# Kernel tuning notes

Hardware: AMD Instinct MI355X
Metric: run time of the kernel (lower is better)

## Reference

```python
import jax, jax.numpy as jnp
import numpy as np

T = 5          # temporal_window_size
B = 512        # batch (graphs per timestep)
NA = 16        # num_agents (nodes per graph)
S = 64         # num_belief_states
A = 16         # action_dim
HID = 64       # hidden_dim per head
H = 4          # num_attn_heads
FD = HID * H   # 256, feature_dim
LAT = 128      # latent_dim
N = B * NA     # total nodes per timestep
FIN = S + A    # node feature dim
NEG_SLOPE = 0.2


def _edge_index():
    i, j = np.meshgrid(np.arange(NA), np.arange(NA), indexing='ij')
    m = i != j
    src_l, dst_l = i[m], j[m]                      # 240 intra-clique edges
    off = (np.arange(B) * NA)[:, None]
    src = (src_l[None] + off).ravel()
    dst = (dst_l[None] + off).ravel()
    loops = np.arange(N)                           # PyG GATConv add_self_loops=True
    src = np.concatenate([src, loops])
    dst = np.concatenate([dst, loops])
    return jnp.asarray(np.stack([src, dst]), dtype=jnp.int64)


def setup_inputs() -> dict:
    key = jax.random.key(0)
    ks = jax.random.split(key, 24)
    xav = lambda k, shp: jax.random.normal(k, shp, jnp.float32) * np.float32(np.sqrt(2.0 / (shp[0] + shp[-1])))
    return {
        'signals': jax.random.normal(ks[0], (T, B, S), jnp.float32),
        'neighbor_actions': jax.random.normal(ks[1], (T, B, NA * A), jnp.float32),
        'lin_w0': xav(ks[2], (FD, FIN)),
        'att_src0': xav(ks[3], (H, HID)),
        'att_dst0': xav(ks[4], (H, HID)),
        'bias0': jnp.zeros((FD,), jnp.float32),
        'lin_w1': xav(ks[5], (FD, FD)),
        'att_src1': xav(ks[6], (H, HID)),
        'att_dst1': xav(ks[7], (H, HID)),
        'bias1': jnp.zeros((FD,), jnp.float32),
        'in_proj_w': xav(ks[8], (3 * FD, FD)),
        'in_proj_b': jnp.zeros((3 * FD,), jnp.float32),
        'out_proj_w': xav(ks[9], (FD, FD)),
        'out_proj_b': jnp.zeros((FD,), jnp.float32),
        'w_mean': xav(ks[10], (LAT, FD)),
        'b_mean': jnp.zeros((LAT,), jnp.float32),
        'w_logvar': xav(ks[11], (LAT, FD)),
        'b_logvar': jnp.zeros((LAT,), jnp.float32),
        'w_belief': xav(ks[12], (S, FD)),
        'b_belief': jnp.zeros((S,), jnp.float32),
        'edge_index': _edge_index(),
    }


def _segment_softmax(e, seg, num_segments):
    # e: [E, T, H]; softmax over edges sharing the same target node.
    m = jax.ops.segment_max(e, seg, num_segments=num_segments)
    e = jnp.exp(e - m[seg])
    s = jax.ops.segment_sum(e, seg, num_segments=num_segments)
    return e / s[seg]


def _gat(x, src, dst, w, a_src, a_dst, b):
    # x: [N, T, Fin] -> [N, T, H*HID]   (PyG GATConv, concat heads)
    xl = jnp.einsum('ntf,of->nto', x, w).reshape(N, T, H, HID)
    e_src = jnp.einsum('nthc,hc->nth', xl, a_src)[src]   # [E, T, H]
    e_dst = jnp.einsum('nthc,hc->nth', xl, a_dst)[dst]
    e = jax.nn.leaky_relu(e_src + e_dst, NEG_SLOPE)
    alpha = _segment_softmax(e, dst, N)                  # per-target softmax
    out = jax.ops.segment_sum(alpha[..., None] * xl[src], dst, num_segments=N)
    return out.reshape(N, T, FD) + b


def reference(signals, neighbor_actions, lin_w0, att_src0, att_dst0, bias0,
              lin_w1, att_src1, att_dst1, bias1, in_proj_w, in_proj_b,
              out_proj_w, out_proj_b, w_mean, b_mean, w_logvar, b_logvar,
              w_belief, b_belief, edge_index):
    # --- _construct_graph (vectorized over time window + batch) ---
    acts = neighbor_actions.reshape(T, B, NA, A)
    beliefs = jnp.zeros((T, B, NA, S), signals.dtype).at[:, :, 0, :].set(signals)
    nodes = jnp.concatenate([beliefs, acts], -1).reshape(T, N, FIN)
    nodes = jnp.transpose(nodes, (1, 0, 2))              # [N, T, FIN]
    src, dst = edge_index[0], edge_index[1]
    x = jax.nn.relu(_gat(nodes, src, dst, lin_w0, att_src0, att_dst0, bias0))
    x = jax.nn.relu(_gat(x, src, dst, lin_w1, att_src1, att_dst1, bias1))
    # --- ego-node sequence: nodes 0, NA, 2*NA, ... ---
    seq = x[::NA]                                        # [B, T, FD]
    # --- temporal MultiheadAttention (batch_first, eval) ---
    qkv = seq @ in_proj_w.T + in_proj_b
    q, k, v = jnp.split(qkv, 3, axis=-1)
    dh = FD // H
    q = q.reshape(B, T, H, dh); k = k.reshape(B, T, H, dh); v = v.reshape(B, T, H, dh)
    scores = jnp.einsum('bqhd,bkhd->bhqk', q, k) / jnp.sqrt(jnp.asarray(dh, seq.dtype))
    # torch float attn_mask is ADDITIVE: mask[i,j]=1 if j<=i else 0
    mask = (jnp.arange(T)[:, None] >= jnp.arange(T)[None, :]).astype(seq.dtype)
    attn = jax.nn.softmax(scores + mask[None, None], axis=-1)
    ctx = jnp.einsum('bhqk,bkhd->bqhd', attn, v).reshape(B, T, FD)
    ctx = ctx @ out_proj_w.T + out_proj_b
    feat = ctx[:, -1]                                    # [B, FD]
    # --- heads ---
    mean = feat @ w_mean.T + b_mean
    logvar = feat @ w_logvar.T + b_logvar
    belief = jax.nn.softmax(feat @ w_belief.T + b_belief, axis=-1)
    return (mean, logvar, belief)
```

## Files before the change

### kernel.cpp

```cpp
#include <hip/hip_runtime.h>
#include <hip/hip_bf16.h>


__device__ __forceinline__ float wave_sum64(float v) {
    #pragma unroll
    for (int off = 32; off > 0; off >>= 1) v += __shfl_xor(v, off, 64);
    return v;
}
__device__ __forceinline__ float wave_max64(float v) {
    #pragma unroll
    for (int off = 32; off > 0; off >>= 1) v = fmaxf(v, __shfl_xor(v, off, 64));
    return v;
}

__global__ __launch_bounds__(256) void k_pre(
    const float* __restrict__ w0, const float* __restrict__ w1,
    const float* __restrict__ wip, const float* __restrict__ wop,
    const float* __restrict__ wm, const float* __restrict__ wlv,
    const float* __restrict__ wb,
    const float* __restrict__ as0, const float* __restrict__ ad0,
    const float* __restrict__ as1, const float* __restrict__ ad1,
    float* __restrict__ tws,
    float* __restrict__ u1, float* __restrict__ ud1,
    float* __restrict__ pa0, float* __restrict__ pd0)
{
    const int tid = threadIdx.x;
    if (blockIdx.x < 1680) {
        int i = blockIdx.x * 256 + tid;
        float v;
        if (i < 16384) {
            int k = i >> 8, n = i & 255;
            v = w0[n * 80 + k];
        } else if (i < 20480) {
            int j = i - 16384; int k = j >> 8, n = j & 255;
            v = w0[n * 80 + 64 + k];
        } else if (i < 86016) {
            int j = i - 20480; int k = j >> 8, n = j & 255;
            v = w1[n * 256 + k];
        } else if (i < 282624) {
            int j = i - 86016; int k = j / 768, n = j - k * 768;
            v = wip[n * 256 + k];
        } else if (i < 348160) {
            int j = i - 282624; int k = j >> 8, n = j & 255;
            v = wop[n * 256 + k];
        } else {
            int j = i - 348160; int k = j / 320, o = j - k * 320;
            if (o < 128)      v = wm[o * 256 + k];
            else if (o < 256) v = wlv[(o - 128) * 256 + k];
            else              v = wb[(o - 256) * 256 + k];
        }
        tws[i] = v;
        return;
    }
    for (int q = 0; q < 4; q++) {
        int idx = q * 256 + tid;
        int h = idx >> 8, k = idx & 255;
        float su = 0.f, sd = 0.f;
        for (int c = 0; c < 64; c++) {
            float wv = w1[(h * 64 + c) * 256 + k];
            su = fmaf(as1[h * 64 + c], wv, su);
            sd = fmaf(ad1[h * 64 + c], wv, sd);
        }
        u1[idx] = su; ud1[idx] = sd;
    }
    if (tid < 64) {
        int h = tid >> 4, k = tid & 15;
        float su = 0.f, sd = 0.f;
        for (int c = 0; c < 64; c++) {
            float wv = w0[(h * 64 + c) * 80 + 64 + k];
            su = fmaf(as0[h * 64 + c], wv, su);
            sd = fmaf(ad0[h * 64 + c], wv, sd);
        }
        pa0[tid] = su; pd0[tid] = sd;
    }
}

__global__ __launch_bounds__(256, 4) void k_gat(
    const float* __restrict__ sig,
    const float* __restrict__ nact,
    const float* __restrict__ W0sT,
    const float* __restrict__ W0aT,
    const float* __restrict__ W1T,
    const float* __restrict__ u1g, const float* __restrict__ ud1g,
    const float* __restrict__ pa0g, const float* __restrict__ pd0g,
    const float* __restrict__ as0, const float* __restrict__ ad0,
    const float* __restrict__ b0, const float* __restrict__ b1,
    float* __restrict__ seqf)
{
    __shared__ __align__(16) char smem[37120];
    float* actL    = (float*)(smem + 0);
    float* sigL    = (float*)(smem + 1024);
    float* u1L     = (float*)(smem + 1280);
    float* ud1L    = (float*)(smem + 5440);
    float* pa0L    = (float*)(smem + 9600);
    float* pd0L    = (float*)(smem + 9856);
    float* es0w    = (float*)(smem + 10112);
    float* ed0w    = (float*)(smem + 10368);
    float* espL    = (float*)(smem + 10624);
    float* es1L    = (float*)(smem + 11648);
    float* edpL    = (float*)(smem + 11904);
    float* alpha1L = (float*)(smem + 11968);
    float* a0L     = (float*)(smem + 12224);
    float* zL      = (float*)(smem + 16320);
    float* x1L     = (float*)(smem + 20480);

    const int tid = threadIdx.x;
    const int bg = blockIdx.x;
    const int b = bg / 5, g = bg - b * 5;
    const int n = tid, w = tid >> 6, lane = tid & 63;

    if (tid < 64) sigL[tid] = sig[(g * 512 + b) * 64 + tid];
    actL[tid] = nact[(g * 512 + b) * 256 + tid];
    #pragma unroll
    for (int q = 0; q < 4; q++) {
        int idx = q * 256 + tid;
        int h = idx >> 8, k = idx & 255;
        u1L[h * 260 + k] = u1g[idx];
        ud1L[h * 260 + k] = ud1g[idx];
    }
    if (tid >= 64 && tid < 128) {
        pa0L[tid - 64] = pa0g[tid - 64];
        pd0L[tid - 64] = pd0g[tid - 64];
    }
    __syncthreads();

    float S = 0.f;
    {
        const float4* sig4 = (const float4*)sigL;
        #pragma unroll
        for (int i = 0; i < 4; i++) {
            float wv[16];
            #pragma unroll
            for (int j = 0; j < 16; j++)
                wv[j] = W0sT[(i * 16 + j) * 256 + n];
            #pragma unroll
            for (int q = 0; q < 4; q++) {
                float4 sv = sig4[i * 4 + q];
                S = fmaf(wv[q * 4 + 0], sv.x, S);
                S = fmaf(wv[q * 4 + 1], sv.y, S);
                S = fmaf(wv[q * 4 + 2], sv.z, S);
                S = fmaf(wv[q * 4 + 3], sv.w, S);
            }
        }
    }
    const float sS = wave_sum64(S * as0[n]);
    const float dS = wave_sum64(S * ad0[n]);

    if (lane < 16) {
        const int m = lane;
        float su = (m == 0) ? sS : 0.f;
        float sd = (m == 0) ? dS : 0.f;
        const float4* act4 = (const float4*)(actL + m * 16);
        const float4* pa4  = (const float4*)(pa0L + w * 16);
        const float4* pd4  = (const float4*)(pd0L + w * 16);
        #pragma unroll
        for (int q = 0; q < 4; q++) {
            float4 av = act4[q], pv = pa4[q], dv = pd4[q];
            su = fmaf(av.x, pv.x, su); su = fmaf(av.y, pv.y, su);
            su = fmaf(av.z, pv.z, su); su = fmaf(av.w, pv.w, su);
            sd = fmaf(av.x, dv.x, sd); sd = fmaf(av.y, dv.y, sd);
            sd = fmaf(av.z, dv.z, sd); sd = fmaf(av.w, dv.w, sd);
        }
        es0w[w * 16 + m] = su;
        ed0w[w * 16 + m] = sd;
    }
    if (lane < 16) {
        const int j = lane;
        float ej = ed0w[w * 16 + j];
        float e[16], m = -1e30f;
        const float4* es4 = (const float4*)(es0w + w * 16);
        #pragma unroll
        for (int s4 = 0; s4 < 4; s4++) {
            float4 ev = es4[s4];
            float x;
            x = ev.x + ej; x = (x >= 0.f) ? x : 0.2f * x; e[s4*4+0] = x; m = fmaxf(m, x);
            x = ev.y + ej; x = (x >= 0.f) ? x : 0.2f * x; e[s4*4+1] = x; m = fmaxf(m, x);
            x = ev.z + ej; x = (x >= 0.f) ? x : 0.2f * x; e[s4*4+2] = x; m = fmaxf(m, x);
            x = ev.w + ej; x = (x >= 0.f) ? x : 0.2f * x; e[s4*4+3] = x; m = fmaxf(m, x);
        }
        float sum = 0.f;
        #pragma unroll
        for (int s = 0; s < 16; s++) { e[s] = __expf(e[s] - m); sum += e[s]; }
        float inv = 1.f / sum;
        float4* a04 = (float4*)(a0L + w * 256 + j * 16);
        #pragma unroll
        for (int s4 = 0; s4 < 4; s4++)
            a04[s4] = make_float4(e[s4 * 4] * inv, e[s4 * 4 + 1] * inv,
                                  e[s4 * 4 + 2] * inv, e[s4 * 4 + 3] * inv);
    }

    float x1r[16];
    {
        float wr[16];
        #pragma unroll
        for (int k = 0; k < 16; k++) wr[k] = W0aT[k * 256 + n];
        const float4* act4 = (const float4*)actL;
        float xl0r[16];
        #pragma unroll
        for (int s = 0; s < 16; s++) {
            float a = 0.f;
            #pragma unroll
            for (int q = 0; q < 4; q++) {
                float4 av = act4[s * 4 + q];
                a = fmaf(av.x, wr[q * 4 + 0], a);
                a = fmaf(av.y, wr[q * 4 + 1], a);
                a = fmaf(av.z, wr[q * 4 + 2], a);
                a = fmaf(av.w, wr[q * 4 + 3], a);
            }
            xl0r[s] = a;
        }
        xl0r[0] += S;
        const float b0v = b0[n];
        const float4* a04 = (const float4*)(a0L + w * 256);
        #pragma unroll
        for (int j = 0; j < 16; j++) {
            float acc = b0v;
            #pragma unroll
            for (int s4 = 0; s4 < 4; s4++) {
                float4 a4 = a04[j * 4 + s4];
                acc = fmaf(a4.x, xl0r[s4 * 4 + 0], acc);
                acc = fmaf(a4.y, xl0r[s4 * 4 + 1], acc);
                acc = fmaf(a4.z, xl0r[s4 * 4 + 2], acc);
                acc = fmaf(a4.w, xl0r[s4 * 4 + 3], acc);
            }
            x1r[j] = fmaxf(acc, 0.f);
            x1L[j * 260 + n] = x1r[j];
        }
    }
    __syncthreads();

    {
        const int m = tid & 15, h = (tid >> 4) & 3, p = tid >> 6;
        const float4* x4p = (const float4*)(x1L + m * 260 + p * 64);
        const float4* u4p = (const float4*)(u1L + h * 260 + p * 64);
        float a = 0.f;
        #pragma unroll
        for (int i = 0; i < 16; i++) {
            float4 xv = x4p[i], uv = u4p[i];
            a = fmaf(xv.x, uv.x, a);
            a = fmaf(xv.y, uv.y, a);
            a = fmaf(xv.z, uv.z, a);
            a = fmaf(xv.w, uv.w, a);
        }
        espL[m * 16 + h * 4 + p] = a;
        if (m == 0) {
            const float4* ud4p = (const float4*)(ud1L + h * 260 + p * 64);
            float ad = 0.f;
            #pragma unroll
            for (int i = 0; i < 16; i++) {
                float4 xv = x4p[i], uv = ud4p[i];
                ad = fmaf(xv.x, uv.x, ad);
                ad = fmaf(xv.y, uv.y, ad);
                ad = fmaf(xv.z, uv.z, ad);
                ad = fmaf(xv.w, uv.w, ad);
            }
            edpL[h * 4 + p] = ad;
        }
    }
    __syncthreads();

    if (w == 0) {
        {
            const int m = lane >> 2, h = lane & 3;
            const float* e = espL + m * 16 + h * 4;
            es1L[m * 4 + h] = e[0] + e[1] + e[2] + e[3];
        }
        if (lane < 4) {
            const int h = lane;
            float ej = edpL[h * 4] + edpL[h * 4 + 1] + edpL[h * 4 + 2] + edpL[h * 4 + 3];
            float e[16], m = -1e30f;
            #pragma unroll
            for (int s = 0; s < 16; s++) {
                float x = es1L[s * 4 + h] + ej;
                x = (x >= 0.f) ? x : 0.2f * x;
                e[s] = x; m = fmaxf(m, x);
            }
            float sum = 0.f;
            #pragma unroll
            for (int s = 0; s < 16; s++) { e[s] = __expf(e[s] - m); sum += e[s]; }
            float inv = 1.f / sum;
            #pragma unroll
            for (int s = 0; s < 16; s++) alpha1L[h * 16 + s] = e[s] * inv;
        }
    }
    __syncthreads();

    {
        const float4* a14 = (const float4*)alpha1L;
        #pragma unroll
        for (int hh = 0; hh < 4; hh++) {
            float zv = 0.f;
            #pragma unroll
            for (int s4 = 0; s4 < 4; s4++) {
                float4 a4 = a14[hh * 4 + s4];
                zv = fmaf(a4.x, x1r[s4 * 4 + 0], zv);
                zv = fmaf(a4.y, x1r[s4 * 4 + 1], zv);
                zv = fmaf(a4.z, x1r[s4 * 4 + 2], zv);
                zv = fmaf(a4.w, x1r[s4 * 4 + 3], zv);
            }
            zL[hh * 260 + n] = zv;
        }
    }
    __syncthreads();

    {
        const float4* zh = (const float4*)(zL + w * 260);
        float acc = b1[n];
        for (int i = 0; i < 16; i++) {
            float wv[16];
            #pragma unroll
            for (int j = 0; j < 16; j++)
                wv[j] = W1T[(i * 16 + j) * 256 + n];
            #pragma unroll
            for (int q = 0; q < 4; q++) {
                float4 z4 = zh[i * 4 + q];
                acc = fmaf(wv[q * 4 + 0], z4.x, acc);
                acc = fmaf(wv[q * 4 + 1], z4.y, acc);
                acc = fmaf(wv[q * 4 + 2], z4.z, acc);
                acc = fmaf(wv[q * 4 + 3], z4.w, acc);
            }
        }
        seqf[bg * 256 + n] = fmaxf(acc, 0.f);
    }
}

__global__ __launch_bounds__(768) void k_stage2(
    const float* __restrict__ seqf,
    const float* __restrict__ wipT,
    const float* __restrict__ bip,
    const float* __restrict__ wopT,
    const float* __restrict__ bop,
    const float* __restrict__ whT,
    const float* __restrict__ bm, const float* __restrict__ blv,
    const float* __restrict__ bb,
    float* __restrict__ out)
{
    __shared__ float sseq[2][5][256];
    __shared__ float kL[2][5][256], vL[2][5][256], qL[2][256];
    __shared__ float ctxL[2][256], featL[2][256];
    __shared__ float beliefL[2][64];
    const int tid = threadIdx.x;
    const int b0 = blockIdx.x * 2;

    {
        float* sflat = &sseq[0][0][0];
        for (int i = tid; i < 2560; i += 768)
            sflat[i] = seqf[b0 * 1280 + i];
    }
    __syncthreads();

    {
        const int kind = tid >> 8, n = tid & 255;
        if (kind == 0) {
            float a0 = 0.f, a1 = 0.f;
            for (int k = 0; k < 256; k++) {
                float wv = wipT[k * 768 + n];
                a0 = fmaf(sseq[0][4][k], wv, a0);
                a1 = fmaf(sseq[1][4][k], wv, a1);
            }
            float bv = bip[n];
            qL[0][n] = a0 + bv; qL[1][n] = a1 + bv;
        } else {
            const float* wcol = wipT + kind * 256 + n;
            float acc[2][5];
            #pragma unroll
            for (int gb = 0; gb < 2; gb++)
                #pragma unroll
                for (int t = 0; t < 5; t++) acc[gb][t] = 0.f;
            for (int k = 0; k < 256; k++) {
                float wv = wcol[k * 768];
                #pragma unroll
                for (int gb = 0; gb < 2; gb++) {
                    #pragma unroll
                    for (int t = 0; t < 5; t++)
                        acc[gb][t] = fmaf(sseq[gb][t][k], wv, acc[gb][t]);
                }
            }
            float bv = bip[kind * 256 + n];
            float* dst = (kind == 1) ? &kL[0][0][0] : &vL[0][0][0];
            #pragma unroll
            for (int gb = 0; gb < 2; gb++)
                #pragma unroll
                for (int t = 0; t < 5; t++)
                    dst[gb * 1280 + t * 256 + n] = acc[gb][t] + bv;
        }
    }
    __syncthreads();

    if (tid < 512) {
        const int gb = tid >> 8, col = tid & 255;
        float q4 = qL[gb][col];
        float sc[5];
        #pragma unroll
        for (int t = 0; t < 5; t++)
            sc[t] = wave_sum64(q4 * kL[gb][t][col]) * 0.125f;
        float m = sc[0];
        #pragma unroll
        for (int t = 1; t < 5; t++) m = fmaxf(m, sc[t]);
        float p[5], sum = 0.f;
        #pragma unroll
        for (int t = 0; t < 5; t++) { p[t] = __expf(sc[t] - m); sum += p[t]; }
        float inv = 1.f / sum, cv = 0.f;
        #pragma unroll
        for (int t = 0; t < 5; t++) cv = fmaf(p[t], vL[gb][t][col], cv);
        ctxL[gb][col] = cv * inv;
    }
    __syncthreads();

    if (tid < 512) {
        const int gb = tid >> 8, n = tid & 255;
        float acc = 0.f;
        for (int k = 0; k < 256; k++)
            acc = fmaf(ctxL[gb][k], wopT[k * 256 + n], acc);
        featL[gb][n] = acc + bop[n];
    }
    __syncthreads();

    if (tid < 640) {
        const int gb = tid / 320, j = tid - gb * 320;
        float acc = 0.f;
        for (int k = 0; k < 256; k++)
            acc = fmaf(featL[gb][k], whT[k * 320 + j], acc);
        if (j < 128) {
            out[(b0 + gb) * 128 + j] = acc + bm[j];
        } else if (j < 256) {
            out[65536 + (b0 + gb) * 128 + (j - 128)] = acc + blv[j - 128];
        } else {
            beliefL[gb][j - 256] = acc + bb[j - 256];
        }
    }
    __syncthreads();

    if (tid < 128) {
        int gb = tid >> 6, lane = tid & 63;
        float lg = beliefL[gb][lane];
        float m = wave_max64(lg);
        float e = __expf(lg - m);
        float s = wave_sum64(e);
        out[131072 + (b0 + gb) * 64 + lane] = e / s;
    }
}

extern "C" void kernel_launch(void* const* d_in, const int* in_sizes, int n_in,
                              void* d_out, int out_size, void* d_ws, size_t ws_size,
                              hipStream_t stream) {
    const float* sig  = (const float*)d_in[0];
    const float* nact = (const float*)d_in[1];
    const float* w0   = (const float*)d_in[2];
    const float* as0  = (const float*)d_in[3];
    const float* ad0  = (const float*)d_in[4];
    const float* b0   = (const float*)d_in[5];
    const float* w1   = (const float*)d_in[6];
    const float* as1  = (const float*)d_in[7];
    const float* ad1  = (const float*)d_in[8];
    const float* b1   = (const float*)d_in[9];
    const float* wip  = (const float*)d_in[10];
    const float* bip  = (const float*)d_in[11];
    const float* wop  = (const float*)d_in[12];
    const float* bop  = (const float*)d_in[13];
    const float* wm   = (const float*)d_in[14];
    const float* bm   = (const float*)d_in[15];
    const float* wlv  = (const float*)d_in[16];
    const float* blv  = (const float*)d_in[17];
    const float* wb   = (const float*)d_in[18];
    const float* bb   = (const float*)d_in[19];

    float* ws    = (float*)d_ws;
    float* seqf  = ws;
    float* tws   = ws + 655360;
    float* W0sT  = tws;
    float* W0aT  = tws + 16384;
    float* W1T   = tws + 20480;
    float* wipT  = tws + 86016;
    float* wopT  = tws + 282624;
    float* whT   = tws + 348160;
    float* u1    = ws + 1085440;
    float* ud1   = ws + 1086464;
    float* pa0   = ws + 1087488;
    float* pd0   = ws + 1087552;

    k_pre   <<<1681, 256, 0, stream>>>(w0, w1, wip, wop, wm, wlv, wb,
                                       as0, ad0, as1, ad1,
                                       tws, u1, ud1, pa0, pd0);
    k_gat   <<<2560, 256, 0, stream>>>(sig, nact, W0sT, W0aT, W1T,
                                       u1, ud1, pa0, pd0, as0, ad0, b0, b1, seqf);
    k_stage2<<<256, 768, 0, stream>>>(seqf, wipT, bip, wopT, bop, whT,
                                      bm, blv, bb, (float*)d_out);
}
```

Measured before the change: 199.6 us.

## Pack weights as float4 k-quads and vectorize GAT and stage2 matvecs

The pre-transpose kernel now writes weights in a packed layout where each output column holds four consecutive k values contiguously. All matvec loops in k_gat and k_stage2 can then use 128-bit loads and float4 shared-memory reads. k_gat also drops the shared-memory staging of u1/ud1/pa0/pd0, prefetches weights into registers before the first barrier and W1 before the second, and runs the small softmaxes across four lanes with shuffles. Occupancy hint rises to 5 blocks per CU with less LDS, at the cost of higher register pressure from the prefetched float4 arrays.

```diff
diff --git a/kernel.cpp b/kernel.cpp
--- a/kernel.cpp
+++ b/kernel.cpp
@@ -27,29 +27,35 @@
     const int tid = threadIdx.x;
     if (blockIdx.x < 1680) {
         int i = blockIdx.x * 256 + tid;
-        float v;
+        float v; int d;
         if (i < 16384) {
-            int k = i >> 8, n = i & 255;
-            v = w0[n * 80 + k];
+            int k = i & 63, nn = i >> 6;
+            v = w0[nn * 80 + k];
+            d = (k >> 2) * 1024 + nn * 4 + (k & 3);
         } else if (i < 20480) {
-            int j = i - 16384; int k = j >> 8, n = j & 255;
-            v = w0[n * 80 + 64 + k];
+            int j = i - 16384; int k = j & 15, nn = j >> 4;
+            v = w0[nn * 80 + 64 + k];
+            d = 16384 + (k >> 2) * 1024 + nn * 4 + (k & 3);
         } else if (i < 86016) {
-            int j = i - 20480; int k = j >> 8, n = j & 255;
-            v = w1[n * 256 + k];
+            int j = i - 20480; int k = j & 255, nn = j >> 8;
+            v = w1[nn * 256 + k];
+            d = 20480 + (k >> 2) * 1024 + nn * 4 + (k & 3);
         } else if (i < 282624) {
-            int j = i - 86016; int k = j / 768, n = j - k * 768;
-            v = wip[n * 256 + k];
+            int j = i - 86016; int k = j & 255, nn = j >> 8;
+            v = wip[nn * 256 + k];
+            d = 86016 + (k >> 2) * 3072 + nn * 4 + (k & 3);
         } else if (i < 348160) {
-            int j = i - 282624; int k = j >> 8, n = j & 255;
-            v = wop[n * 256 + k];
+            int j = i - 282624; int k = j & 255, nn = j >> 8;
+            v = wop[nn * 256 + k];
+            d = 282624 + (k >> 2) * 1024 + nn * 4 + (k & 3);
         } else {
-            int j = i - 348160; int k = j / 320, o = j - k * 320;
+            int j = i - 348160; int k = j & 255, o = j >> 8;
             if (o < 128)      v = wm[o * 256 + k];
             else if (o < 256) v = wlv[(o - 128) * 256 + k];
             else              v = wb[(o - 256) * 256 + k];
-        }
-        tws[i] = v;
+            d = 348160 + (k >> 2) * 1280 + o * 4 + (k & 3);
+        }
+        tws[d] = v;
         return;
     }
     for (int q = 0; q < 4; q++) {
@@ -75,125 +81,121 @@
     }
 }
 
-__global__ __launch_bounds__(256, 4) void k_gat(
+__global__ __launch_bounds__(256, 5) void k_gat(
     const float* __restrict__ sig,
     const float* __restrict__ nact,
-    const float* __restrict__ W0sT,
-    const float* __restrict__ W0aT,
-    const float* __restrict__ W1T,
+    const float* __restrict__ W0sPK,
+    const float* __restrict__ W0aPK,
+    const float* __restrict__ W1PK,
     const float* __restrict__ u1g, const float* __restrict__ ud1g,
     const float* __restrict__ pa0g, const float* __restrict__ pd0g,
     const float* __restrict__ as0, const float* __restrict__ ad0,
     const float* __restrict__ b0, const float* __restrict__ b1,
     float* __restrict__ seqf)
 {
-    __shared__ __align__(16) char smem[37120];
+    __shared__ __align__(16) char smem[28288];
     float* actL    = (float*)(smem + 0);
     float* sigL    = (float*)(smem + 1024);
-    float* u1L     = (float*)(smem + 1280);
-    float* ud1L    = (float*)(smem + 5440);
-    float* pa0L    = (float*)(smem + 9600);
-    float* pd0L    = (float*)(smem + 9856);
-    float* es0w    = (float*)(smem + 10112);
-    float* ed0w    = (float*)(smem + 10368);
-    float* espL    = (float*)(smem + 10624);
-    float* es1L    = (float*)(smem + 11648);
-    float* edpL    = (float*)(smem + 11904);
-    float* alpha1L = (float*)(smem + 11968);
-    float* a0L     = (float*)(smem + 12224);
-    float* zL      = (float*)(smem + 16320);
-    float* x1L     = (float*)(smem + 20480);
+    float* es0w    = (float*)(smem + 1280);
+    float* ed0w    = (float*)(smem + 1536);
+    float* espL    = (float*)(smem + 1792);
+    float* es1L    = (float*)(smem + 2816);
+    float* edpL    = (float*)(smem + 3072);
+    float* alpha1L = (float*)(smem + 3136);
+    float* a0L     = (float*)(smem + 3392);
+    float* zL      = (float*)(smem + 7488);
+    float* x1L     = (float*)(smem + 11648);
 
     const int tid = threadIdx.x;
     const int bg = blockIdx.x;
     const int b = bg / 5, g = bg - b * 5;
     const int n = tid, w = tid >> 6, lane = tid & 63;
 
-    if (tid < 64) sigL[tid] = sig[(g * 512 + b) * 64 + tid];
-    actL[tid] = nact[(g * 512 + b) * 256 + tid];
+    const float4* W0sPK4 = (const float4*)W0sPK;
+
+    float4 wv0[8];
     #pragma unroll
-    for (int q = 0; q < 4; q++) {
-        int idx = q * 256 + tid;
-        int h = idx >> 8, k = idx & 255;
-        u1L[h * 260 + k] = u1g[idx];
-        ud1L[h * 260 + k] = ud1g[idx];
-    }
-    if (tid >= 64 && tid < 128) {
-        pa0L[tid - 64] = pa0g[tid - 64];
-        pd0L[tid - 64] = pd0g[tid - 64];
-    }
+    for (int j = 0; j < 8; j++) wv0[j] = W0sPK4[j * 256 + n];
+    float4 wa[4];
+    {
+        const float4* W0aPK4 = (const float4*)W0aPK;
+        #pragma unroll
+        for (int q = 0; q < 4; q++) wa[q] = W0aPK4[q * 256 + n];
+    }
+    const float as0n = as0[n];
+    const float ad0n = ad0[n];
+
+    if (tid < 16)
+        ((float4*)sigL)[tid] = ((const float4*)(sig + (g * 512 + b) * 64))[tid];
+    if (tid < 64)
+        ((float4*)actL)[tid] = ((const float4*)(nact + (g * 512 + b) * 256))[tid];
     __syncthreads();
 
     float S = 0.f;
     {
         const float4* sig4 = (const float4*)sigL;
         #pragma unroll
-        for (int i = 0; i < 4; i++) {
-            float wv[16];
-            #pragma unroll
-            for (int j = 0; j < 16; j++)
-                wv[j] = W0sT[(i * 16 + j) * 256 + n];
-            #pragma unroll
-            for (int q = 0; q < 4; q++) {
-                float4 sv = sig4[i * 4 + q];
-                S = fmaf(wv[q * 4 + 0], sv.x, S);
-                S = fmaf(wv[q * 4 + 1], sv.y, S);
-                S = fmaf(wv[q * 4 + 2], sv.z, S);
-                S = fmaf(wv[q * 4 + 3], sv.w, S);
-            }
-        }
-    }
-    const float sS = wave_sum64(S * as0[n]);
-    const float dS = wave_sum64(S * ad0[n]);
-
-    if (lane < 16) {
-        const int m = lane;
-        float su = (m == 0) ? sS : 0.f;
-        float sd = (m == 0) ? dS : 0.f;
-        const float4* act4 = (const float4*)(actL + m * 16);
-        const float4* pa4  = (const float4*)(pa0L + w * 16);
-        const float4* pd4  = (const float4*)(pd0L + w * 16);
-        #pragma unroll
-        for (int q = 0; q < 4; q++) {
-            float4 av = act4[q], pv = pa4[q], dv = pd4[q];
-            su = fmaf(av.x, pv.x, su); su = fmaf(av.y, pv.y, su);
-            su = fmaf(av.z, pv.z, su); su = fmaf(av.w, pv.w, su);
-            sd = fmaf(av.x, dv.x, sd); sd = fmaf(av.y, dv.y, sd);
-            sd = fmaf(av.z, dv.z, sd); sd = fmaf(av.w, dv.w, sd);
-        }
-        es0w[w * 16 + m] = su;
-        ed0w[w * 16 + m] = sd;
-    }
-    if (lane < 16) {
-        const int j = lane;
-        float ej = ed0w[w * 16 + j];
-        float e[16], m = -1e30f;
-        const float4* es4 = (const float4*)(es0w + w * 16);
-        #pragma unroll
-        for (int s4 = 0; s4 < 4; s4++) {
-            float4 ev = es4[s4];
-            float x;
-            x = ev.x + ej; x = (x >= 0.f) ? x : 0.2f * x; e[s4*4+0] = x; m = fmaxf(m, x);
-            x = ev.y + ej; x = (x >= 0.f) ? x : 0.2f * x; e[s4*4+1] = x; m = fmaxf(m, x);
-            x = ev.z + ej; x = (x >= 0.f) ? x : 0.2f * x; e[s4*4+2] = x; m = fmaxf(m, x);
-            x = ev.w + ej; x = (x >= 0.f) ? x : 0.2f * x; e[s4*4+3] = x; m = fmaxf(m, x);
-        }
-        float sum = 0.f;
-        #pragma unroll
-        for (int s = 0; s < 16; s++) { e[s] = __expf(e[s] - m); sum += e[s]; }
-        float inv = 1.f / sum;
-        float4* a04 = (float4*)(a0L + w * 256 + j * 16);
-        #pragma unroll
-        for (int s4 = 0; s4 < 4; s4++)
-            a04[s4] = make_float4(e[s4 * 4] * inv, e[s4 * 4 + 1] * inv,
-                                  e[s4 * 4 + 2] * inv, e[s4 * 4 + 3] * inv);
+        for (int j = 0; j < 8; j++) {
+            float4 sv = sig4[j];
+            S = fmaf(wv0[j].x, sv.x, S);
+            S = fmaf(wv0[j].y, sv.y, S);
+            S = fmaf(wv0[j].z, sv.z, S);
+            S = fmaf(wv0[j].w, sv.w, S);
+        }
+        float4 wv1[8];
+        #pragma unroll
+        for (int j = 0; j < 8; j++) wv1[j] = W0sPK4[(8 + j) * 256 + n];
+        #pragma unroll
+        for (int j = 0; j < 8; j++) {
+            float4 sv = sig4[8 + j];
+            S = fmaf(wv1[j].x, sv.x, S);
+            S = fmaf(wv1[j].y, sv.y, S);
+            S = fmaf(wv1[j].z, sv.z, S);
+            S = fmaf(wv1[j].w, sv.w, S);
+        }
+    }
+    const int m3 = lane >> 2, q3 = lane & 3;
+    const float4 pv = ((const float4*)(pa0g + w * 16))[q3];
+    const float4 dv = ((const float4*)(pd0g + w * 16))[q3];
+
+    const float sS = wave_sum64(S * as0n);
+    const float dS = wave_sum64(S * ad0n);
+
+    {
+        const float4 av = ((const float4*)(actL + m3 * 16))[q3];
+        float su = av.x * pv.x;
+        su = fmaf(av.y, pv.y, su); su = fmaf(av.z, pv.z, su); su = fmaf(av.w, pv.w, su);
+        float sd = av.x * dv.x;
+        sd = fmaf(av.y, dv.y, sd); sd = fmaf(av.z, dv.z, sd); sd = fmaf(av.w, dv.w, sd);
+        su += __shfl_xor(su, 1, 64); su += __shfl_xor(su, 2, 64);
+        sd += __shfl_xor(sd, 1, 64); sd += __shfl_xor(sd, 2, 64);
+        if (q3 == 0) {
+            es0w[w * 16 + m3] = su + ((m3 == 0) ? sS : 0.f);
+            ed0w[w * 16 + m3] = sd + ((m3 == 0) ? dS : 0.f);
+        }
+    }
+    {
+        const int j = lane >> 2, q = lane & 3;
+        const float ej = ed0w[w * 16 + j];
+        const float4 ev = ((const float4*)(es0w + w * 16))[q];
+        float e0 = ev.x + ej; e0 = (e0 >= 0.f) ? e0 : 0.2f * e0;
+        float e1 = ev.y + ej; e1 = (e1 >= 0.f) ? e1 : 0.2f * e1;
+        float e2 = ev.z + ej; e2 = (e2 >= 0.f) ? e2 : 0.2f * e2;
+        float e3 = ev.w + ej; e3 = (e3 >= 0.f) ? e3 : 0.2f * e3;
+        float mx = fmaxf(fmaxf(e0, e1), fmaxf(e2, e3));
+        mx = fmaxf(mx, __shfl_xor(mx, 1, 64));
+        mx = fmaxf(mx, __shfl_xor(mx, 2, 64));
+        e0 = __expf(e0 - mx); e1 = __expf(e1 - mx);
+        e2 = __expf(e2 - mx); e3 = __expf(e3 - mx);
+        float s = e0 + e1 + e2 + e3;
+        s += __shfl_xor(s, 1, 64); s += __shfl_xor(s, 2, 64);
+        float inv = 1.f / s;
+        ((float4*)(a0L + w * 256 + j * 16))[q] =
+            make_float4(e0 * inv, e1 * inv, e2 * inv, e3 * inv);
     }
 
     float x1r[16];
     {
-        float wr[16];
-        #pragma unroll
-        for (int k = 0; k < 16; k++) wr[k] = W0aT[k * 256 + n];
         const float4* act4 = (const float4*)actL;
         float xl0r[16];
         #pragma unroll
@@ -202,10 +204,10 @@
             #pragma unroll
             for (int q = 0; q < 4; q++) {
                 float4 av = act4[s * 4 + q];
-                a = fmaf(av.x, wr[q * 4 + 0], a);
-                a = fmaf(av.y, wr[q * 4 + 1], a);
-                a = fmaf(av.z, wr[q * 4 + 2], a);
-                a = fmaf(av.w, wr[q * 4 + 3], a);
+                a = fmaf(av.x, wa[q].x, a);
+                a = fmaf(av.y, wa[q].y, a);
+                a = fmaf(av.z, wa[q].z, a);
+                a = fmaf(av.w, wa[q].w, a);
             }
             xl0r[s] = a;
         }
@@ -232,7 +234,7 @@
     {
         const int m = tid & 15, h = (tid >> 4) & 3, p = tid >> 6;
         const float4* x4p = (const float4*)(x1L + m * 260 + p * 64);
-        const float4* u4p = (const float4*)(u1L + h * 260 + p * 64);
+        const float4* u4p = ((const float4*)u1g) + h * 64 + p * 16;
         float a = 0.f;
         #pragma unroll
         for (int i = 0; i < 16; i++) {
@@ -244,7 +246,7 @@
         }
         espL[m * 16 + h * 4 + p] = a;
         if (m == 0) {
-            const float4* ud4p = (const float4*)(ud1L + h * 260 + p * 64);
+            const float4* ud4p = ((const float4*)ud1g) + h * 64 + p * 16;
             float ad = 0.f;
             #pragma unroll
             for (int i = 0; i < 16; i++) {
@@ -261,30 +263,39 @@
 
     if (w == 0) {
         {
-            const int m = lane >> 2, h = lane & 3;
-            const float* e = espL + m * 16 + h * 4;
-            es1L[m * 4 + h] = e[0] + e[1] + e[2] + e[3];
-        }
-        if (lane < 4) {
-            const int h = lane;
+            const int m2 = lane >> 2, h = lane & 3;
+            const float* e = espL + m2 * 16 + h * 4;
+            es1L[m2 * 4 + h] = e[0] + e[1] + e[2] + e[3];
+        }
+        if (lane < 16) {
+            const int h = lane >> 2, q = lane & 3;
             float ej = edpL[h * 4] + edpL[h * 4 + 1] + edpL[h * 4 + 2] + edpL[h * 4 + 3];
-            float e[16], m = -1e30f;
-            #pragma unroll
-            for (int s = 0; s < 16; s++) {
-                float x = es1L[s * 4 + h] + ej;
+            float e[4]; float mx = -1e30f;
+            #pragma unroll
+            for (int r = 0; r < 4; r++) {
+                float x = es1L[(q * 4 + r) * 4 + h] + ej;
                 x = (x >= 0.f) ? x : 0.2f * x;
-                e[s] = x; m = fmaxf(m, x);
-            }
-            float sum = 0.f;
-            #pragma unroll
-            for (int s = 0; s < 16; s++) { e[s] = __expf(e[s] - m); sum += e[s]; }
-            float inv = 1.f / sum;
-            #pragma unroll
-            for (int s = 0; s < 16; s++) alpha1L[h * 16 + s] = e[s] * inv;
-        }
-    }
-    __syncthreads();
-
+                e[r] = x; mx = fmaxf(mx, x);
+            }
+            mx = fmaxf(mx, __shfl_xor(mx, 1, 64));
+            mx = fmaxf(mx, __shfl_xor(mx, 2, 64));
+            float s = 0.f;
+            #pragma unroll
+            for (int r = 0; r < 4; r++) { e[r] = __expf(e[r] - mx); s += e[r]; }
+            s += __shfl_xor(s, 1, 64);
+            s += __shfl_xor(s, 2, 64);
+            float inv = 1.f / s;
+            ((float4*)(alpha1L + h * 16 + q * 4))[0] =
+                make_float4(e[0] * inv, e[1] * inv, e[2] * inv, e[3] * inv);
+        }
+    }
+    __syncthreads();
+
+    const float4* W1PK4 = (const float4*)W1PK;
+    float4 w1pf[8];
+    #pragma unroll
+    for (int j = 0; j < 8; j++) w1pf[j] = W1PK4[j * 256 + n];
+    const float b1v = b1[n];
     {
         const float4* a14 = (const float4*)alpha1L;
         #pragma unroll
@@ -305,19 +316,27 @@
 
     {
         const float4* zh = (const float4*)(zL + w * 260);
-        float acc = b1[n];
-        for (int i = 0; i < 16; i++) {
-            float wv[16];
-            #pragma unroll
-            for (int j = 0; j < 16; j++)
-                wv[j] = W1T[(i * 16 + j) * 256 + n];
-            #pragma unroll
-            for (int q = 0; q < 4; q++) {
-                float4 z4 = zh[i * 4 + q];
-                acc = fmaf(wv[q * 4 + 0], z4.x, acc);
-                acc = fmaf(wv[q * 4 + 1], z4.y, acc);
-                acc = fmaf(wv[q * 4 + 2], z4.z, acc);
-                acc = fmaf(wv[q * 4 + 3], z4.w, acc);
+        float acc = b1v;
+        #pragma unroll
+        for (int j = 0; j < 8; j++) {
+            float4 z4 = zh[j];
+            acc = fmaf(w1pf[j].x, z4.x, acc);
+            acc = fmaf(w1pf[j].y, z4.y, acc);
+            acc = fmaf(w1pf[j].z, z4.z, acc);
+            acc = fmaf(w1pf[j].w, z4.w, acc);
+        }
+        #pragma unroll
+        for (int io = 1; io < 8; io++) {
+            float4 wv[8];
+            #pragma unroll
+            for (int j = 0; j < 8; j++) wv[j] = W1PK4[(io * 8 + j) * 256 + n];
+            #pragma unroll
+            for (int j = 0; j < 8; j++) {
+                float4 z4 = zh[io * 8 + j];
+                acc = fmaf(wv[j].x, z4.x, acc);
+                acc = fmaf(wv[j].y, z4.y, acc);
+                acc = fmaf(wv[j].z, z4.z, acc);
+                acc = fmaf(wv[j].w, z4.w, acc);
             }
         }
         seqf[bg * 256 + n] = fmaxf(acc, 0.f);
@@ -326,11 +345,11 @@
 
 __global__ __launch_bounds__(768) void k_stage2(
     const float* __restrict__ seqf,
-    const float* __restrict__ wipT,
+    const float* __restrict__ wipPK,
     const float* __restrict__ bip,
-    const float* __restrict__ wopT,
+    const float* __restrict__ wopPK,
     const float* __restrict__ bop,
-    const float* __restrict__ whT,
+    const float* __restrict__ whPK,
     const float* __restrict__ bm, const float* __restrict__ blv,
     const float* __restrict__ bb,
     float* __restrict__ out)
@@ -343,37 +362,45 @@
     const int b0 = blockIdx.x * 2;
 
     {
-        float* sflat = &sseq[0][0][0];
-        for (int i = tid; i < 2560; i += 768)
-            sflat[i] = seqf[b0 * 1280 + i];
+        float4* sflat = (float4*)&sseq[0][0][0];
+        const float4* src = (const float4*)(seqf + b0 * 1280);
+        if (tid < 640) sflat[tid] = src[tid];
     }
     __syncthreads();
 
     {
         const int kind = tid >> 8, n = tid & 255;
+        const float4* wPK = (const float4*)wipPK + tid;
         if (kind == 0) {
+            const float4* s0 = (const float4*)&sseq[0][4][0];
+            const float4* s1 = (const float4*)&sseq[1][4][0];
             float a0 = 0.f, a1 = 0.f;
-            for (int k = 0; k < 256; k++) {
-                float wv = wipT[k * 768 + n];
-                a0 = fmaf(sseq[0][4][k], wv, a0);
-                a1 = fmaf(sseq[1][4][k], wv, a1);
+            #pragma unroll 8
+            for (int k4 = 0; k4 < 64; k4++) {
+                float4 wv = wPK[k4 * 768];
+                float4 x0 = s0[k4], x1 = s1[k4];
+                a0 = fmaf(x0.x, wv.x, a0); a0 = fmaf(x0.y, wv.y, a0);
+                a0 = fmaf(x0.z, wv.z, a0); a0 = fmaf(x0.w, wv.w, a0);
+                a1 = fmaf(x1.x, wv.x, a1); a1 = fmaf(x1.y, wv.y, a1);
+                a1 = fmaf(x1.z, wv.z, a1); a1 = fmaf(x1.w, wv.w, a1);
             }
             float bv = bip[n];
             qL[0][n] = a0 + bv; qL[1][n] = a1 + bv;
         } else {
-            const float* wcol = wipT + kind * 256 + n;
-            float acc[2][5];
-            #pragma unroll
-            for (int gb = 0; gb < 2; gb++)
-                #pragma unroll
-                for (int t = 0; t < 5; t++) acc[gb][t] = 0.f;
-            for (int k = 0; k < 256; k++) {
-                float wv = wcol[k * 768];
+            float acc[2][5] = {{0.f,0.f,0.f,0.f,0.f},{0.f,0.f,0.f,0.f,0.f}};
+            #pragma unroll 4
+            for (int k4 = 0; k4 < 64; k4++) {
+                float4 wv = wPK[k4 * 768];
                 #pragma unroll
                 for (int gb = 0; gb < 2; gb++) {
                     #pragma unroll
-                    for (int t = 0; t < 5; t++)
-                        acc[gb][t] = fmaf(sseq[gb][t][k], wv, acc[gb][t]);
+                    for (int t = 0; t < 5; t++) {
+                        float4 sv = ((const float4*)&sseq[gb][t][0])[k4];
+                        float a = acc[gb][t];
+                        a = fmaf(sv.x, wv.x, a); a = fmaf(sv.y, wv.y, a);
+                        a = fmaf(sv.z, wv.z, a); a = fmaf(sv.w, wv.w, a);
+                        acc[gb][t] = a;
+                    }
                 }
             }
             float bv = bip[kind * 256 + n];
@@ -409,18 +436,30 @@
 
     if (tid < 512) {
         const int gb = tid >> 8, n = tid & 255;
+        const float4* wPK = (const float4*)wopPK + n;
+        const float4* c4 = (const float4*)&ctxL[gb][0];
         float acc = 0.f;
-        for (int k = 0; k < 256; k++)
-            acc = fmaf(ctxL[gb][k], wopT[k * 256 + n], acc);
+        #pragma unroll 8
+        for (int k4 = 0; k4 < 64; k4++) {
+            float4 wv = wPK[k4 * 256], cv = c4[k4];
+            acc = fmaf(cv.x, wv.x, acc); acc = fmaf(cv.y, wv.y, acc);
+            acc = fmaf(cv.z, wv.z, acc); acc = fmaf(cv.w, wv.w, acc);
+        }
         featL[gb][n] = acc + bop[n];
     }
     __syncthreads();
 
     if (tid < 640) {
         const int gb = tid / 320, j = tid - gb * 320;
+        const float4* wPK = (const float4*)whPK + j;
+        const float4* f4 = (const float4*)&featL[gb][0];
         float acc = 0.f;
-        for (int k = 0; k < 256; k++)
-            acc = fmaf(featL[gb][k], whT[k * 320 + j], acc);
+        #pragma unroll 8
+        for (int k4 = 0; k4 < 64; k4++) {
+            float4 wv = wPK[k4 * 320], fv = f4[k4];
+            acc = fmaf(fv.x, wv.x, acc); acc = fmaf(fv.y, wv.y, acc);
+            acc = fmaf(fv.z, wv.z, acc); acc = fmaf(fv.w, wv.w, acc);
+        }
         if (j < 128) {
             out[(b0 + gb) * 128 + j] = acc + bm[j];
         } else if (j < 256) {
@@ -468,12 +507,12 @@
     float* ws    = (float*)d_ws;
     float* seqf  = ws;
     float* tws   = ws + 655360;
-    float* W0sT  = tws;
-    float* W0aT  = tws + 16384;
-    float* W1T   = tws + 20480;
-    float* wipT  = tws + 86016;
-    float* wopT  = tws + 282624;
-    float* whT   = tws + 348160;
+    float* W0sPK = tws;
+    float* W0aPK = tws + 16384;
+    float* W1PK  = tws + 20480;
+    float* wipPK = tws + 86016;
+    float* wopPK = tws + 282624;
+    float* whPK  = tws + 348160;
     float* u1    = ws + 1085440;
     float* ud1   = ws + 1086464;
     float* pa0   = ws + 1087488;
@@ -482,8 +521,8 @@
     k_pre   <<<1681, 256, 0, stream>>>(w0, w1, wip, wop, wm, wlv, wb,
                                        as0, ad0, as1, ad1,
                                        tws, u1, ud1, pa0, pd0);
-    k_gat   <<<2560, 256, 0, stream>>>(sig, nact, W0sT, W0aT, W1T,
+    k_gat   <<<2560, 256, 0, stream>>>(sig, nact, W0sPK, W0aPK, W1PK,
                                        u1, ud1, pa0, pd0, as0, ad0, b0, b1, seqf);
-    k_stage2<<<256, 768, 0, stream>>>(seqf, wipT, bip, wopT, bop, whT,
+    k_stage2<<<256, 768, 0, stream>>>(seqf, wipPK, bip, wopPK, bop, whPK,
                                       bm, blv, bb, (float*)d_out);
 }
```

Result: faster. 194.6 us (-2.5%).
